# Optimization experiments

Measured on AMD Instinct MI355X. Metric: run time of the kernel, lower is better.

Reference implementation:

```python
import jax, jax.numpy as jnp
import numpy as np

N, E, R, C_IN, C_OUT = 100000, 1600000, 6, 8, 16
EPS = 1e-8


def setup_inputs() -> dict:
    key = jax.random.key(0)
    ks = jax.random.split(key, 6)
    x = jax.random.normal(ks[0], (N, C_IN), dtype=jnp.float32)
    supp_edges = jax.random.randint(ks[1], (E, 2), 0, N, dtype=jnp.int64)
    # (E, R, 2): real/imag of precomputed complex stencil (radial bins x transport x weights)
    lift_sten = jax.random.normal(ks[2], (E, R, 2), dtype=jnp.float32) * 0.1
    # TransField learned radial weights (real) and per-channel phase offsets (ftype=1)
    weight = jax.random.normal(ks[3], (R, C_IN, C_OUT), dtype=jnp.float32) * np.float32(1.0 / np.sqrt(R * C_IN))
    offset = jax.random.normal(ks[4], (C_IN, C_OUT), dtype=jnp.float32)
    # TangentNonLin per-channel magnitude bias (modReLU)
    bias = jax.random.normal(ks[5], (C_OUT,), dtype=jnp.float32) * 0.1
    return {"x": x, "supp_edges": supp_edges, "lift_sten": lift_sten,
            "weight": weight, "offset": offset, "bias": bias}


def reference(x, supp_edges, lift_sten, weight, offset, bias):
    src = supp_edges[:, 0]  # j: source
    dst = supp_edges[:, 1]  # i: target
    sten = jax.lax.complex(lift_sten[..., 0], lift_sten[..., 1])          # (E, R) complex64
    xj = x[src]                                                           # (E, Cin) gather
    # per-edge complex message over radial bins and input channels
    msg = sten[:, :, None] * xj[:, None, :].astype(sten.dtype)            # (E, R, Cin)
    agg = jax.ops.segment_sum(msg, dst, num_segments=N)                   # (N, R, Cin)
    # learned filter: real radial weights with per-channel phase offsets exp(i*theta)
    phase = jax.lax.complex(jnp.cos(offset), jnp.sin(offset))             # (Cin, Cout)
    filt = weight.astype(phase.dtype) * phase[None, :, :]                 # (R, Cin, Cout)
    y = jnp.einsum('nrc,rco->no', agg, filt)                              # (N, Cout) complex
    # TangentNonLin: modReLU on magnitude, phase preserved
    mag = jnp.abs(y)
    scale = jax.nn.relu(mag + bias[None, :]) / (mag + EPS)
    y = y * scale.astype(y.dtype)
    # return real/imag stacked for a real-valued output tensor (N, Cout, 2)
    return jnp.stack([jnp.real(y), jnp.imag(y)], axis=-1)
```

## Files before the change

kernel.cpp:

```cpp
#include <hip/hip_runtime.h>
#include <hip/hip_fp16.h>
#include <math.h>

#define N_NODES 100000
#define N_EDGES 1600000
#define RR      6
#define CIN     8
#define COUT    16
#define EPS     1e-8f

#define NBLK_A  512
#define ABLOCK  1024
#define CHUNK   (N_EDGES / NBLK_A)
#define NBUCK   391
#define RECCAP  4608
#define QCAP    1536

#define LDS_SPAY   0
#define LDS_SHDR   75000
#define LDS_SBKT   87500
#define LDS_CNT    93752
#define LDS_TOTAL  100032

__device__ inline unsigned int pack_f16(float a, float b) {
    __half2 h = __floats2half2_rn(a, b);
    return *(unsigned int*)&h;
}

__global__ __launch_bounds__(ABLOCK)
void partition_kernel(const int* __restrict__ edges,
                      const float* __restrict__ sten,
                      int* __restrict__ gcur,
                      unsigned int* __restrict__ hdr,
                      unsigned int* __restrict__ pay) {
    extern __shared__ char smem[];
    uint2*          spay = (uint2*)(smem + LDS_SPAY);
    unsigned int*   shdr = (unsigned int*)(smem + LDS_SHDR);
    unsigned short* sbkt = (unsigned short*)(smem + LDS_SBKT);
    int* cnt   = (int*)(smem + LDS_CNT);
    int* cur   = cnt + NBUCK;
    int* base  = cur + NBUCK;
    int* gbase = base + NBUCK;

    int tid = threadIdx.x;
    int blk = blockIdx.x;
    int e0 = blk * CHUNK;

    for (int i = tid; i < NBUCK; i += ABLOCK) { cnt[i] = 0; cur[i] = 0; }
    __syncthreads();

    for (int i = tid; i < CHUNK; i += ABLOCK) {
        int2 ed = ((const int2*)edges)[e0 + i];
        atomicAdd(&cnt[ed.y >> 8], 1);
    }
    __syncthreads();

    if (tid < 64) {
        int lane = tid;
        int off = 0;
        for (int c = 0; c < NBUCK; c += 64) {
            int idx = c + lane;
            int v = (idx < NBUCK) ? cnt[idx] : 0;
            int orig = v;
#pragma unroll
            for (int d = 1; d < 64; d <<= 1) {
                int t = __shfl_up(v, d);
                if (lane >= d) v += t;
            }
            if (idx < NBUCK) base[idx] = off + v - orig;
            off += __shfl(v, 63);
        }
    }
    __syncthreads();

    for (int b = tid; b < NBUCK; b += ABLOCK) {
        int c = cnt[b];
        gbase[b] = (c > 0) ? atomicAdd(&gcur[b], c) : 0;
    }
    __syncthreads();

    for (int i = tid; i < CHUNK; i += ABLOCK) {
        int e = e0 + i;
        int2 ed = ((const int2*)edges)[e];
        int b = ed.y >> 8;
        int p = base[b] + atomicAdd(&cur[b], 1);
        sbkt[p] = (unsigned short)b;
        shdr[p] = ((unsigned int)ed.x << 8) | (unsigned int)(ed.y & 255);
        const float4* sp = (const float4*)(sten + (size_t)e * 12);
        float4 s0 = sp[0], s1 = sp[1], s2 = sp[2];
        uint2* dp = spay + p * 3;
        dp[0] = (uint2){ pack_f16(s0.x, s0.y), pack_f16(s0.z, s0.w) };
        dp[1] = (uint2){ pack_f16(s1.x, s1.y), pack_f16(s1.z, s1.w) };
        dp[2] = (uint2){ pack_f16(s2.x, s2.y), pack_f16(s2.z, s2.w) };
    }
    __syncthreads();

    for (int p = tid; p < CHUNK; p += ABLOCK) {
        int b = (int)sbkt[p];
        int rel = p - base[b];
        long long slot = (long long)gbase[b] + rel;
        if (slot < RECCAP) {
            size_t rs = (size_t)b * RECCAP + slot;
            hdr[rs] = shdr[p];
            const uint2* sp = spay + p * 3;
            uint2 w0 = sp[0], w1 = sp[1], w2 = sp[2];
            unsigned int* dp = pay + rs * 6;
            *(uint2*)(dp + 0) = w0;
            *(uint2*)(dp + 2) = w1;
            *(uint2*)(dp + 4) = w2;
        }
    }
}

__global__ __launch_bounds__(256, 6)
void bucket_kernel(const float* __restrict__ x,
                   const float* __restrict__ weight,
                   const float* __restrict__ offset,
                   const float* __restrict__ bias,
                   const int* __restrict__ gcur,
                   const unsigned int* __restrict__ hdr,
                   const unsigned int* __restrict__ pay,
                   float* __restrict__ out) {
    __shared__ unsigned int idxs[QCAP];
    __shared__ int cnt[64], nbase[64], cur2[64];
    __shared__ float fre[RR * CIN * COUT];
    __shared__ float fim[RR * CIN * COUT];
    __shared__ float bsh[COUT];

    int tid = threadIdx.x;
    int b   = blockIdx.x >> 2;
    int q   = blockIdx.x & 3;

    for (int i = tid; i < RR * CIN * COUT; i += 256) {
        int co = i % (CIN * COUT);
        float w = weight[i], off = offset[co];
        fre[i] = w * cosf(off);
        fim[i] = w * sinf(off);
    }
    if (tid < COUT) bsh[tid] = bias[tid];
    if (tid < 64) { cnt[tid] = 0; cur2[tid] = 0; }
    __syncthreads();

    int T = gcur[b];
    if (T > RECCAP) T = RECCAP;

    const unsigned int* hslice = hdr + (size_t)b * RECCAP;

    for (int j = tid; j < T; j += 256) {
        unsigned int h = hslice[j];
        int d = (int)(h & 255u);
        if ((d >> 6) == q) atomicAdd(&cnt[d & 63], 1);
    }
    __syncthreads();

    if (tid < 64) {
        int v = cnt[tid];
        int orig = v;
#pragma unroll
        for (int d = 1; d < 64; d <<= 1) {
            int t = __shfl_up(v, d);
            if (tid >= d) v += t;
        }
        nbase[tid] = v - orig;
    }
    __syncthreads();

    for (int j = tid; j < T; j += 256) {
        unsigned int h = hslice[j];
        int d = (int)(h & 255u);
        if ((d >> 6) == q) {
            int dl = d & 63;
            int pos = nbase[dl] + atomicAdd(&cur2[dl], 1);
            if (pos < QCAP)
                idxs[pos] = ((h >> 8) << 13) | (unsigned int)j;
        }
    }
    __syncthreads();

    int local = tid >> 2;
    int n = b * 256 + q * 64 + local;
    int l = tid & 3;
    if (n >= N_NODES) return;

    int deg  = cnt[local];
    int base = nbase[local];
    if (base + deg > QCAP) deg = (base < QCAP) ? (QCAP - base) : 0;

    float ar[RR][2] = {};
    float ai[RR][2] = {};

    uint2 p0 = {}, p1 = {}, p2 = {};
    float2 xv = {};
    if (deg > 0) {
        unsigned int pk = idxs[base];
        int j   = (int)(pk & 8191u);
        int src = (int)(pk >> 13);
        const unsigned int* pp = pay + ((size_t)b * RECCAP + j) * 6;
        p0 = *(const uint2*)(pp + 0);
        p1 = *(const uint2*)(pp + 2);
        p2 = *(const uint2*)(pp + 4);
        xv = *(const float2*)(x + (size_t)src * CIN + 2 * l);
    }
    for (int k = 0; k < deg; ++k) {
        uint2 q0 = {}, q1 = {}, q2 = {};
        float2 nx = {};
        if (k + 1 < deg) {
            unsigned int pk = idxs[base + k + 1];
            int j   = (int)(pk & 8191u);
            int src = (int)(pk >> 13);
            const unsigned int* pp = pay + ((size_t)b * RECCAP + j) * 6;
            q0 = *(const uint2*)(pp + 0);
            q1 = *(const uint2*)(pp + 2);
            q2 = *(const uint2*)(pp + 4);
            nx = *(const float2*)(x + (size_t)src * CIN + 2 * l);
        }
        unsigned int wv[6] = {p0.x, p0.y, p1.x, p1.y, p2.x, p2.y};
#pragma unroll
        for (int r = 0; r < RR; ++r) {
            __half2 h = *(__half2*)&wv[r];
            float sre = __half2float(__low2half(h));
            float sim = __half2float(__high2half(h));
            ar[r][0] = fmaf(sre, xv.x, ar[r][0]);
            ar[r][1] = fmaf(sre, xv.y, ar[r][1]);
            ai[r][0] = fmaf(sim, xv.x, ai[r][0]);
            ai[r][1] = fmaf(sim, xv.y, ai[r][1]);
        }
        p0 = q0; p1 = q1; p2 = q2; xv = nx;
    }

    float yr[COUT], yi[COUT];
#pragma unroll
    for (int o = 0; o < COUT; ++o) { yr[o] = 0.f; yi[o] = 0.f; }
#pragma unroll
    for (int r = 0; r < RR; ++r) {
#pragma unroll
        for (int j = 0; j < 2; ++j) {
            int c = 2 * l + j;
            float are = ar[r][j], aim = ai[r][j];
            const float* fr = &fre[(r * CIN + c) * COUT];
            const float* fi = &fim[(r * CIN + c) * COUT];
#pragma unroll
            for (int o = 0; o < COUT; ++o) {
                yr[o] = fmaf(are, fr[o], yr[o]);
                yr[o] = fmaf(-aim, fi[o], yr[o]);
                yi[o] = fmaf(are, fi[o], yi[o]);
                yi[o] = fmaf(aim, fr[o], yi[o]);
            }
        }
    }
#pragma unroll
    for (int o = 0; o < COUT; ++o) {
        yr[o] += __shfl_xor(yr[o], 1);
        yr[o] += __shfl_xor(yr[o], 2);
        yi[o] += __shfl_xor(yi[o], 1);
        yi[o] += __shfl_xor(yi[o], 2);
    }
    float tmp[8];
    int ob = 4 * l;
#pragma unroll
    for (int j = 0; j < 4; ++j) {
        int o = ob + j;
        float re = yr[o], im = yi[o];
        float mag = sqrtf(re * re + im * im);
        float sc = fmaxf(mag + bsh[o], 0.f) / (mag + EPS);
        tmp[2 * j]     = re * sc;
        tmp[2 * j + 1] = im * sc;
    }
    float4* op = (float4*)(out + (size_t)n * 2 * COUT + 8 * l);
    op[0] = ((const float4*)tmp)[0];
    op[1] = ((const float4*)tmp)[1];
}

extern "C" void kernel_launch(void* const* d_in, const int* in_sizes, int n_in,
                              void* d_out, int out_size, void* d_ws, size_t ws_size,
                              hipStream_t stream) {
    const float* x      = (const float*)d_in[0];
    const int*   edges  = (const int*)d_in[1];
    const float* sten   = (const float*)d_in[2];
    const float* weight = (const float*)d_in[3];
    const float* offset = (const float*)d_in[4];
    const float* bias   = (const float*)d_in[5];
    float* out = (float*)d_out;

    int* gcur = (int*)d_ws;
    unsigned int* hdr = (unsigned int*)((char*)d_ws + 4096);
    unsigned int* pay = hdr + (size_t)NBUCK * RECCAP;

    static int lds_inited = 0;
    if (!lds_inited) {
        (void)hipFuncSetAttribute((const void*)partition_kernel,
                                  hipFuncAttributeMaxDynamicSharedMemorySize,
                                  LDS_TOTAL);
        lds_inited = 1;
    }

    (void)hipMemsetAsync(gcur, 0, sizeof(int) * NBUCK, stream);

    partition_kernel<<<NBLK_A, ABLOCK, LDS_TOTAL, stream>>>(edges, sten, gcur, hdr, pay);
    bucket_kernel<<<NBUCK * 4, 256, 0, stream>>>(x, weight, offset, bias,
                                                 gcur, hdr, pay, out);
}
```

Baseline: 222.0 us.

## Use 128-node buckets with one block per bucket and stage payload in LDS

Destination buckets shrink from 256 to 128 nodes, and each bucket is handled by a single 512-thread block. Previously four blocks each rescanned the whole 256-node header list and kept only a quarter of it. The bucket's fp16 stencil payload is now copied into LDS with coalesced loads, so the per-edge loop reads from shared memory instead of doing scattered global reads. The bucket kernel uses about 72KB of dynamic LDS, which limits how many blocks fit per CU. The per-bucket capacity clamp is also tightened, so high-degree overflow relies on the 2304-slot cap.

```diff
diff --git a/kernel.cpp b/kernel.cpp
--- a/kernel.cpp
+++ b/kernel.cpp
@@ -12,15 +12,25 @@
 #define NBLK_A  512
 #define ABLOCK  1024
 #define CHUNK   (N_EDGES / NBLK_A)
-#define NBUCK   391
-#define RECCAP  4608
-#define QCAP    1536
+
+#define NKEY    782
+#define QCAP3   2304
 
 #define LDS_SPAY   0
 #define LDS_SHDR   75000
 #define LDS_SBKT   87500
 #define LDS_CNT    93752
-#define LDS_TOTAL  100032
+#define LDS_TOTAL  106368
+
+#define BLDS_SPAY  0
+#define BLDS_IDXS  55296
+#define BLDS_FRE   64512
+#define BLDS_FIM   67584
+#define BLDS_CNT   70656
+#define BLDS_NBASE 71168
+#define BLDS_CUR2  71680
+#define BLDS_BSH   72192
+#define BLDS_TOTAL 72320
 
 __device__ inline unsigned int pack_f16(float a, float b) {
     __half2 h = __floats2half2_rn(a, b);
@@ -38,42 +48,42 @@
     unsigned int*   shdr = (unsigned int*)(smem + LDS_SHDR);
     unsigned short* sbkt = (unsigned short*)(smem + LDS_SBKT);
     int* cnt   = (int*)(smem + LDS_CNT);
-    int* cur   = cnt + NBUCK;
-    int* base  = cur + NBUCK;
-    int* gbase = base + NBUCK;
+    int* cur   = cnt + NKEY;
+    int* base  = cur + NKEY;
+    int* gbase = base + NKEY;
 
     int tid = threadIdx.x;
     int blk = blockIdx.x;
     int e0 = blk * CHUNK;
 
-    for (int i = tid; i < NBUCK; i += ABLOCK) { cnt[i] = 0; cur[i] = 0; }
+    for (int i = tid; i < NKEY; i += ABLOCK) { cnt[i] = 0; cur[i] = 0; }
     __syncthreads();
 
     for (int i = tid; i < CHUNK; i += ABLOCK) {
         int2 ed = ((const int2*)edges)[e0 + i];
-        atomicAdd(&cnt[ed.y >> 8], 1);
+        atomicAdd(&cnt[ed.y >> 7], 1);
     }
     __syncthreads();
 
     if (tid < 64) {
         int lane = tid;
         int off = 0;
-        for (int c = 0; c < NBUCK; c += 64) {
+        for (int c = 0; c < NKEY; c += 64) {
             int idx = c + lane;
-            int v = (idx < NBUCK) ? cnt[idx] : 0;
+            int v = (idx < NKEY) ? cnt[idx] : 0;
             int orig = v;
 #pragma unroll
             for (int d = 1; d < 64; d <<= 1) {
                 int t = __shfl_up(v, d);
                 if (lane >= d) v += t;
             }
-            if (idx < NBUCK) base[idx] = off + v - orig;
+            if (idx < NKEY) base[idx] = off + v - orig;
             off += __shfl(v, 63);
         }
     }
     __syncthreads();
 
-    for (int b = tid; b < NBUCK; b += ABLOCK) {
+    for (int b = tid; b < NKEY; b += ABLOCK) {
         int c = cnt[b];
         gbase[b] = (c > 0) ? atomicAdd(&gcur[b], c) : 0;
     }
@@ -82,7 +92,7 @@
     for (int i = tid; i < CHUNK; i += ABLOCK) {
         int e = e0 + i;
         int2 ed = ((const int2*)edges)[e];
-        int b = ed.y >> 8;
+        int b = ed.y >> 7;
         int p = base[b] + atomicAdd(&cur[b], 1);
         sbkt[p] = (unsigned short)b;
         shdr[p] = ((unsigned int)ed.x << 8) | (unsigned int)(ed.y & 255);
@@ -99,8 +109,8 @@
         int b = (int)sbkt[p];
         int rel = p - base[b];
         long long slot = (long long)gbase[b] + rel;
-        if (slot < RECCAP) {
-            size_t rs = (size_t)b * RECCAP + slot;
+        if (slot < QCAP3) {
+            size_t rs = (size_t)b * QCAP3 + slot;
             hdr[rs] = shdr[p];
             const uint2* sp = spay + p * 3;
             uint2 w0 = sp[0], w1 = sp[1], w2 = sp[2];
@@ -112,7 +122,7 @@
     }
 }
 
-__global__ __launch_bounds__(256, 6)
+__global__ __launch_bounds__(512, 4)
 void bucket_kernel(const float* __restrict__ x,
                    const float* __restrict__ weight,
                    const float* __restrict__ offset,
@@ -121,70 +131,78 @@
                    const unsigned int* __restrict__ hdr,
                    const unsigned int* __restrict__ pay,
                    float* __restrict__ out) {
-    __shared__ unsigned int idxs[QCAP];
-    __shared__ int cnt[64], nbase[64], cur2[64];
-    __shared__ float fre[RR * CIN * COUT];
-    __shared__ float fim[RR * CIN * COUT];
-    __shared__ float bsh[COUT];
+    extern __shared__ char smem[];
+    uint2*        spay  = (uint2*)(smem + BLDS_SPAY);
+    unsigned int* idxs  = (unsigned int*)(smem + BLDS_IDXS);
+    float*        fre   = (float*)(smem + BLDS_FRE);
+    float*        fim   = (float*)(smem + BLDS_FIM);
+    int*          cnt   = (int*)(smem + BLDS_CNT);
+    int*          nbase = (int*)(smem + BLDS_NBASE);
+    int*          cur2  = (int*)(smem + BLDS_CUR2);
+    float*        bsh   = (float*)(smem + BLDS_BSH);
 
     int tid = threadIdx.x;
-    int b   = blockIdx.x >> 2;
-    int q   = blockIdx.x & 3;
-
-    for (int i = tid; i < RR * CIN * COUT; i += 256) {
+    int key = blockIdx.x;
+
+    for (int i = tid; i < RR * CIN * COUT; i += 512) {
         int co = i % (CIN * COUT);
         float w = weight[i], off = offset[co];
         fre[i] = w * cosf(off);
         fim[i] = w * sinf(off);
     }
     if (tid < COUT) bsh[tid] = bias[tid];
-    if (tid < 64) { cnt[tid] = 0; cur2[tid] = 0; }
-    __syncthreads();
-
-    int T = gcur[b];
-    if (T > RECCAP) T = RECCAP;
-
-    const unsigned int* hslice = hdr + (size_t)b * RECCAP;
-
-    for (int j = tid; j < T; j += 256) {
+    if (tid < 128) { cnt[tid] = 0; cur2[tid] = 0; }
+
+    int T = gcur[key];
+    if (T > QCAP3) T = QCAP3;
+
+    const unsigned int* hslice = hdr + (size_t)key * QCAP3;
+
+    {
+        const uint2* psrc = (const uint2*)(pay + (size_t)key * QCAP3 * 6);
+        int tw = T * 3;
+        for (int i = tid; i < tw; i += 512) spay[i] = psrc[i];
+    }
+
+    for (int j = tid; j < T; j += 512) {
         unsigned int h = hslice[j];
-        int d = (int)(h & 255u);
-        if ((d >> 6) == q) atomicAdd(&cnt[d & 63], 1);
-    }
-    __syncthreads();
-
-    if (tid < 64) {
+        atomicAdd(&cnt[h & 127u], 1);
+    }
+    __syncthreads();
+
+    if (tid < 128) {
+        int lane = tid & 63;
+        int half = tid >> 6;
         int v = cnt[tid];
         int orig = v;
 #pragma unroll
         for (int d = 1; d < 64; d <<= 1) {
             int t = __shfl_up(v, d);
-            if (tid >= d) v += t;
+            if (lane >= d) v += t;
         }
         nbase[tid] = v - orig;
-    }
-    __syncthreads();
-
-    for (int j = tid; j < T; j += 256) {
+        if (lane == 63 && half == 0) cur2[127] = v;
+    }
+    __syncthreads();
+    if (tid >= 64 && tid < 128) nbase[tid] += cur2[127];
+    if (tid == 127) cur2[127] = 0;
+    __syncthreads();
+
+    for (int j = tid; j < T; j += 512) {
         unsigned int h = hslice[j];
-        int d = (int)(h & 255u);
-        if ((d >> 6) == q) {
-            int dl = d & 63;
-            int pos = nbase[dl] + atomicAdd(&cur2[dl], 1);
-            if (pos < QCAP)
-                idxs[pos] = ((h >> 8) << 13) | (unsigned int)j;
-        }
+        int d = (int)(h & 127u);
+        int pos = nbase[d] + atomicAdd(&cur2[d], 1);
+        idxs[pos] = ((h >> 8) << 12) | (unsigned int)j;
     }
     __syncthreads();
 
     int local = tid >> 2;
-    int n = b * 256 + q * 64 + local;
+    int n = key * 128 + local;
     int l = tid & 3;
     if (n >= N_NODES) return;
 
     int deg  = cnt[local];
     int base = nbase[local];
-    if (base + deg > QCAP) deg = (base < QCAP) ? (QCAP - base) : 0;
 
     float ar[RR][2] = {};
     float ai[RR][2] = {};
@@ -193,12 +211,10 @@
     float2 xv = {};
     if (deg > 0) {
         unsigned int pk = idxs[base];
-        int j   = (int)(pk & 8191u);
-        int src = (int)(pk >> 13);
-        const unsigned int* pp = pay + ((size_t)b * RECCAP + j) * 6;
-        p0 = *(const uint2*)(pp + 0);
-        p1 = *(const uint2*)(pp + 2);
-        p2 = *(const uint2*)(pp + 4);
+        int j   = (int)(pk & 4095u);
+        int src = (int)(pk >> 12);
+        const uint2* pp = spay + j * 3;
+        p0 = pp[0]; p1 = pp[1]; p2 = pp[2];
         xv = *(const float2*)(x + (size_t)src * CIN + 2 * l);
     }
     for (int k = 0; k < deg; ++k) {
@@ -206,20 +222,18 @@
         float2 nx = {};
         if (k + 1 < deg) {
             unsigned int pk = idxs[base + k + 1];
-            int j   = (int)(pk & 8191u);
-            int src = (int)(pk >> 13);
-            const unsigned int* pp = pay + ((size_t)b * RECCAP + j) * 6;
-            q0 = *(const uint2*)(pp + 0);
-            q1 = *(const uint2*)(pp + 2);
-            q2 = *(const uint2*)(pp + 4);
+            int j   = (int)(pk & 4095u);
+            int src = (int)(pk >> 12);
+            const uint2* pp = spay + j * 3;
+            q0 = pp[0]; q1 = pp[1]; q2 = pp[2];
             nx = *(const float2*)(x + (size_t)src * CIN + 2 * l);
         }
         unsigned int wv[6] = {p0.x, p0.y, p1.x, p1.y, p2.x, p2.y};
 #pragma unroll
         for (int r = 0; r < RR; ++r) {
-            __half2 h = *(__half2*)&wv[r];
-            float sre = __half2float(__low2half(h));
-            float sim = __half2float(__high2half(h));
+            __half2 hh = *(__half2*)&wv[r];
+            float sre = __half2float(__low2half(hh));
+            float sim = __half2float(__high2half(hh));
             ar[r][0] = fmaf(sre, xv.x, ar[r][0]);
             ar[r][1] = fmaf(sre, xv.y, ar[r][1]);
             ai[r][0] = fmaf(sim, xv.x, ai[r][0]);
@@ -283,20 +297,23 @@
     float* out = (float*)d_out;
 
     int* gcur = (int*)d_ws;
-    unsigned int* hdr = (unsigned int*)((char*)d_ws + 4096);
-    unsigned int* pay = hdr + (size_t)NBUCK * RECCAP;
+    unsigned int* hdr = (unsigned int*)((char*)d_ws + 8192);
+    unsigned int* pay = hdr + (size_t)NKEY * QCAP3;
 
     static int lds_inited = 0;
     if (!lds_inited) {
         (void)hipFuncSetAttribute((const void*)partition_kernel,
                                   hipFuncAttributeMaxDynamicSharedMemorySize,
                                   LDS_TOTAL);
+        (void)hipFuncSetAttribute((const void*)bucket_kernel,
+                                  hipFuncAttributeMaxDynamicSharedMemorySize,
+                                  BLDS_TOTAL);
         lds_inited = 1;
     }
 
-    (void)hipMemsetAsync(gcur, 0, sizeof(int) * NBUCK, stream);
+    (void)hipMemsetAsync(gcur, 0, sizeof(int) * NKEY, stream);
 
     partition_kernel<<<NBLK_A, ABLOCK, LDS_TOTAL, stream>>>(edges, sten, gcur, hdr, pay);
-    bucket_kernel<<<NBUCK * 4, 256, 0, stream>>>(x, weight, offset, bias,
-                                                 gcur, hdr, pay, out);
+    bucket_kernel<<<NKEY, 512, BLDS_TOTAL, stream>>>(x, weight, offset, bias,
+                                                     gcur, hdr, pay, out);
 }
```

Measured after the change: 239.2 us. +7.7%, slower.
